# Performance work log

Measured on AMD Instinct MI355X. Metric: run time of the kernel, lower is better.

The kernel has to match this reference:

```python
import jax, jax.numpy as jnp
import numpy as np

N_NODES = 50000
N_EDGES = 800000
IN_FEATS = 128
OUT_FEATS = 64


def setup_inputs() -> dict:
    key = jax.random.key(0)
    k1, k2, k3, k4, k5, k6 = jax.random.split(key, 6)
    feat = jax.random.normal(k1, (N_NODES, IN_FEATS), dtype=jnp.float32)
    edge_src = jax.random.randint(k2, (N_EDGES,), 0, N_NODES, dtype=jnp.int64)
    edge_dst = jax.random.randint(k3, (N_EDGES,), 0, N_NODES, dtype=jnp.int64)
    eweight = jax.random.uniform(k4, (N_EDGES,), dtype=jnp.float32)
    W = jax.random.normal(k5, (OUT_FEATS, IN_FEATS), dtype=jnp.float32) * (1.0 / np.sqrt(IN_FEATS))
    b = jax.random.normal(k6, (OUT_FEATS,), dtype=jnp.float32) * 0.01
    return {"feat": feat, "edge_src": edge_src, "edge_dst": edge_dst,
            "eweight": eweight, "W": W, "b": b}


def reference(feat, edge_src, edge_dst, eweight, W, b):
    # Linear: [N, in] @ [in, out] + [out]
    h = jnp.einsum('ni,oi->no', feat, W) + b
    # u_mul_e: gather src features, scale by per-edge weight -> [E, out]
    m = h[edge_src] * eweight[:, None]
    # sum reduce over dst -> [N, out]
    out = jax.ops.segment_sum(m, edge_dst, num_segments=N_NODES)
    return out
```

## Files before the change

### kernel.cpp

```cpp
#include <hip/hip_runtime.h>

#define IN_FEATS 128
#define OUT_FEATS 64
#define TM 64
#define ALD 136
#define BW_LOG 6
#define BWIDTH 64
#define MAX_NB 1024
#define SE_PER_BLK 2048
#define MAX_BUCKET 3072

typedef short bf16x8 __attribute__((ext_vector_type(8)));
typedef float f32x4 __attribute__((ext_vector_type(4)));

__device__ inline unsigned short f2bf(float f) {
    unsigned u = __float_as_uint(f);
    u += 0x7FFFu + ((u >> 16) & 1u);
    return (unsigned short)(u >> 16);
}
__device__ inline float bf2f_lo(unsigned v) { return __uint_as_float(v << 16); }
__device__ inline float bf2f_hi(unsigned v) { return __uint_as_float(v & 0xFFFF0000u); }
__device__ inline ushort4 cvt4(float4 t) {
    ushort4 s; s.x = f2bf(t.x); s.y = f2bf(t.y); s.z = f2bf(t.z); s.w = f2bf(t.w);
    return s;
}

__global__ __launch_bounds__(256) void coarse_hist(
    const int* __restrict__ edst, int* __restrict__ ghist, int n_edges, int nb)
{
    __shared__ int hist[MAX_NB];
    const int tid = threadIdx.x;
    for (int i = tid; i < nb; i += 256) hist[i] = 0;
    __syncthreads();

    const int n4 = n_edges >> 2;
    const int4* ed4 = (const int4*)edst;
    for (int i = blockIdx.x * 256 + tid; i < n4; i += gridDim.x * 256) {
        int4 d = ed4[i];
        atomicAdd(&hist[d.x >> BW_LOG], 1);
        atomicAdd(&hist[d.y >> BW_LOG], 1);
        atomicAdd(&hist[d.z >> BW_LOG], 1);
        atomicAdd(&hist[d.w >> BW_LOG], 1);
    }
    if (blockIdx.x == 0 && tid < (n_edges & 3))
        atomicAdd(&hist[edst[n4 * 4 + tid] >> BW_LOG], 1);
    __syncthreads();
    for (int i = tid; i < nb; i += 256)
        if (hist[i]) atomicAdd(&ghist[i], hist[i]);
}

__global__ __launch_bounds__(256) void coarse_scan(
    const int* __restrict__ ghist, int* __restrict__ goff,
    int* __restrict__ gcur, int nb)
{
    __shared__ int wsum[4];
    __shared__ int wpre[4];
    const int tid  = threadIdx.x;
    const int lane = tid & 63;
    const int wv   = tid >> 6;
    int i0 = tid * 4;
    int v[4];
    int s = 0;
#pragma unroll
    for (int j = 0; j < 4; ++j) v[j] = (i0 + j < nb) ? ghist[i0 + j] : 0;
#pragma unroll
    for (int j = 0; j < 4; ++j) { int t = v[j]; v[j] = s; s += t; }
    int inc = s;
    for (int off = 1; off < 64; off <<= 1) {
        int t = __shfl_up(inc, off, 64);
        if (lane >= off) inc += t;
    }
    int wexcl = inc - s;
    if (lane == 63) wsum[wv] = inc;
    __syncthreads();
    if (tid == 0) {
        int a = 0;
        for (int k = 0; k < 4; ++k) { wpre[k] = a; a += wsum[k]; }
    }
    __syncthreads();
    int tbase = wpre[wv] + wexcl;
#pragma unroll
    for (int j = 0; j < 4; ++j) {
        int idx = i0 + j;
        if (idx < nb) { int e = tbase + v[j]; goff[idx] = e; gcur[idx] = e; }
    }
    if (tid == 0) goff[nb] = wpre[3] + wsum[3];
}

__global__ __launch_bounds__(256) void stage_linear(
    const float* __restrict__ feat, const float* __restrict__ W,
    const float* __restrict__ b, unsigned short* __restrict__ h,
    const int* __restrict__ esrc, const int* __restrict__ edst,
    const float* __restrict__ ew, int* __restrict__ gcur,
    int2* __restrict__ gstage, int n_nodes, int n_edges, int nb, int nstage)
{
    __shared__ union {
        struct { unsigned short As[TM * ALD]; unsigned short Ws[OUT_FEATS * ALD]; } lin;
        struct { int cnt[MAX_NB]; int base[MAX_NB]; } st;
    } sm;
    const int tid = threadIdx.x;

    if ((int)blockIdx.x < nstage) {
        int* cnt  = sm.st.cnt;
        int* base = sm.st.base;
        for (int i = tid; i < nb; i += 256) cnt[i] = 0;
        __syncthreads();

        const int e0 = blockIdx.x * SE_PER_BLK + tid * 8;
        int dk[8]; int sk[8]; float wk[8]; int bk[8]; int rk[8];
        if (e0 + 7 < n_edges) {
            *((int4*)&dk[0]) = *((const int4*)&edst[e0]);
            *((int4*)&dk[4]) = *((const int4*)&edst[e0 + 4]);
            *((int4*)&sk[0]) = *((const int4*)&esrc[e0]);
            *((int4*)&sk[4]) = *((const int4*)&esrc[e0 + 4]);
            *((float4*)&wk[0]) = *((const float4*)&ew[e0]);
            *((float4*)&wk[4]) = *((const float4*)&ew[e0 + 4]);
#pragma unroll
            for (int i = 0; i < 8; ++i) {
                bk[i] = dk[i] >> BW_LOG;
                rk[i] = atomicAdd(&cnt[bk[i]], 1);
            }
        } else {
#pragma unroll
            for (int i = 0; i < 8; ++i) {
                int e = e0 + i;
                if (e < n_edges) {
                    dk[i] = edst[e]; sk[i] = esrc[e]; wk[i] = ew[e];
                    bk[i] = dk[i] >> BW_LOG;
                    rk[i] = atomicAdd(&cnt[bk[i]], 1);
                } else bk[i] = -1;
            }
        }
        __syncthreads();
        for (int i = tid; i < nb; i += 256) {
            int c = cnt[i];
            base[i] = c ? atomicAdd(&gcur[i], c) : 0;
        }
        __syncthreads();
#pragma unroll
        for (int i = 0; i < 8; ++i) {
            if (bk[i] >= 0)
                gstage[base[bk[i]] + rk[i]] =
                    make_int2(((dk[i] & (BWIDTH - 1)) << 16) | sk[i],
                              __float_as_int(wk[i]));
        }
    } else {
        unsigned short* As = sm.lin.As;
        unsigned short* Ws = sm.lin.Ws;
        const int row0 = ((int)blockIdx.x - nstage) * TM;

        {
            const int c  = tid & 63;
            const int kb = (tid >> 6) * 32;
            const float4* wrow = (const float4*)(W + (size_t)c * IN_FEATS + kb);
#pragma unroll
            for (int i = 0; i < 8; ++i)
                *((ushort4*)&Ws[c * ALD + kb + i * 4]) = cvt4(wrow[i]);
        }
        {
#pragma unroll
            for (int i = 0; i < 8; ++i) {
                int flat = i * 256 + tid;
                int r  = flat >> 5;
                int kc = flat & 31;
                int gr = row0 + r;
                float4 t = (gr < n_nodes)
                    ? ((const float4*)(feat + (size_t)gr * IN_FEATS))[kc]
                    : make_float4(0.f, 0.f, 0.f, 0.f);
                *((ushort4*)&As[r * ALD + kc * 4]) = cvt4(t);
            }
        }
        __syncthreads();

        const int w    = tid >> 6;
        const int lane = tid & 63;
        const int m    = lane & 15;
        const int quad = lane >> 4;
        const int koff = quad * 8;

        f32x4 acc[4];
#pragma unroll
        for (int t = 0; t < 4; ++t) acc[t] = (f32x4){0.f, 0.f, 0.f, 0.f};

#pragma unroll
        for (int chunk = 0; chunk < 4; ++chunk) {
            const int kc = chunk * 32 + koff;
            bf16x8 a = *((const bf16x8*)&As[(w * 16 + m) * ALD + kc]);
#pragma unroll
            for (int t = 0; t < 4; ++t) {
                bf16x8 bfr = *((const bf16x8*)&Ws[(t * 16 + m) * ALD + kc]);
                acc[t] = __builtin_amdgcn_mfma_f32_16x16x32_bf16(a, bfr, acc[t], 0, 0, 0);
            }
        }

#pragma unroll
        for (int t = 0; t < 4; ++t) {
            const int col = t * 16 + m;
            const float bias = b[col];
#pragma unroll
            for (int i = 0; i < 4; ++i) {
                int r = row0 + w * 16 + quad * 4 + i;
                if (r < n_nodes)
                    h[(size_t)r * OUT_FEATS + col] = f2bf(acc[t][i] + bias);
            }
        }
    }
}

__global__ __launch_bounds__(256) void bin_sort(
    int2* __restrict__ gstage, const int* __restrict__ goff,
    int2* __restrict__ seg, int n_nodes, int nb)
{
    __shared__ int2 recs[MAX_BUCKET];
    __shared__ int cnt[BWIDTH];
    __shared__ int cur[BWIDTH];
    const int tid = threadIdx.x;
    const int b   = blockIdx.x;
    const int s0  = goff[b], s1 = goff[b + 1];
    const int m   = s1 - s0;

    if (tid < BWIDTH) cnt[tid] = 0;
    __syncthreads();

    for (int i = tid; i < m; i += 256) {
        int2 r = gstage[s0 + i];
        recs[i] = r;
        atomicAdd(&cnt[(r.x >> 16) & 63], 1);
    }
    __syncthreads();

    if (tid < 64) {
        int v = cnt[tid];
        int inc = v;
        for (int o = 1; o < 64; o <<= 1) {
            int t = __shfl_up(inc, o, 64);
            if (tid >= o) inc += t;
        }
        int excl = inc - v;
        cur[tid] = excl;
        int node = b * BWIDTH + tid;
        if (node < n_nodes) seg[node] = make_int2(s0 + excl, s0 + excl + v);
    }
    __syncthreads();

    for (int i = tid; i < m; i += 256) {
        int2 r = recs[i];
        int pos = atomicAdd(&cur[(r.x >> 16) & 63], 1);
        gstage[s0 + pos] = r;
    }
}

__global__ __launch_bounds__(256) void gather_kernel(
    const unsigned short* __restrict__ h, const int2* __restrict__ seg,
    const int2* __restrict__ perm2, float* __restrict__ out, int n_nodes)
{
    const int wid  = (blockIdx.x * blockDim.x + threadIdx.x) >> 6;
    const int lane = threadIdx.x & 63;
    const int g    = lane >> 5;
    const int f2   = lane & 31;
    const int node = wid * 2 + g;
    const unsigned* h32 = (const unsigned*)h;

    int2 se = (node < n_nodes) ? seg[node] : make_int2(0, 0);
    const int len = se.y - se.x;
    const int olen = __shfl_xor(len, 32, 64);
    const int omax = max(len, olen);

    float a0 = 0.f, a1 = 0.f;
    for (int u = 0; u < omax; u += 8) {
        int2 r[8]; unsigned hv[8];
#pragma unroll
        for (int k = 0; k < 8; ++k) {
            int uk  = u + k;
            int pos = (uk < len) ? (se.x + uk) : (len > 0 ? se.y - 1 : 0);
            r[k] = perm2[pos];
        }
#pragma unroll
        for (int k = 0; k < 8; ++k)
            hv[k] = h32[(size_t)(r[k].x & 0xFFFF) * 32 + f2];
#pragma unroll
        for (int k = 0; k < 8; ++k) {
            float w = (u + k < len) ? __int_as_float(r[k].y) : 0.f;
            a0 += w * bf2f_lo(hv[k]);
            a1 += w * bf2f_hi(hv[k]);
        }
    }
    if (node < n_nodes) {
        float2 o; o.x = a0; o.y = a1;
        *((float2*)&out[(size_t)node * OUT_FEATS + 2 * f2]) = o;
    }
}

__global__ __launch_bounds__(256) void scatter_kernel(
    const unsigned short* __restrict__ h, const int* __restrict__ esrc,
    const int* __restrict__ edst, const float* __restrict__ ew,
    float* __restrict__ out, int n_edges)
{
    const int lane = threadIdx.x & 63;
    const int wave = threadIdx.x >> 6;
    const int stride = gridDim.x * 4;
    for (int e = blockIdx.x * 4 + wave; e < n_edges; e += stride) {
        const int s = esrc[e];
        const int d = edst[e];
        const float w = ew[e];
        atomicAdd(out + (size_t)d * OUT_FEATS + lane,
                  bf2f_lo((unsigned)h[(size_t)s * OUT_FEATS + lane]) * w);
    }
}

extern "C" void kernel_launch(void* const* d_in, const int* in_sizes, int n_in,
                              void* d_out, int out_size, void* d_ws, size_t ws_size,
                              hipStream_t stream) {
    const float* feat = (const float*)d_in[0];
    const int*   esrc = (const int*)d_in[1];
    const int*   edst = (const int*)d_in[2];
    const float* ew   = (const float*)d_in[3];
    const float* W    = (const float*)d_in[4];
    const float* b    = (const float*)d_in[5];
    float* out = (float*)d_out;

    const int n_nodes = in_sizes[0] / IN_FEATS;
    const int n_edges = in_sizes[1];
    const int nb = (n_nodes + BWIDTH - 1) >> BW_LOG;
    const int nlin = (n_nodes + TM - 1) / TM;
    const int nstage = (n_edges + SE_PER_BLK - 1) / SE_PER_BLK;

    char* wsb = (char*)d_ws;
    unsigned short* h = (unsigned short*)wsb;
    size_t off_ghist = (((size_t)n_nodes * OUT_FEATS * sizeof(unsigned short)) + 15) & ~(size_t)15;
    size_t sz_ghist  = (((size_t)nb * sizeof(int)) + 15) & ~(size_t)15;
    size_t off_goff  = off_ghist + sz_ghist;
    size_t sz_goff   = (((size_t)(nb + 1) * sizeof(int)) + 15) & ~(size_t)15;
    size_t off_gcur  = off_goff + sz_goff;
    size_t sz_gcur   = (((size_t)nb * sizeof(int)) + 15) & ~(size_t)15;
    size_t off_seg   = off_gcur + sz_gcur;
    size_t sz_seg    = (((size_t)n_nodes * sizeof(int2)) + 15) & ~(size_t)15;
    size_t off_stage = off_seg + sz_seg;
    size_t needed    = off_stage + (size_t)n_edges * sizeof(int2);

    bool binnable = (nb <= MAX_NB) && (n_nodes < 65536) &&
                    ((size_t)n_edges / (size_t)nb * 2 + 256 <= MAX_BUCKET);

    if (ws_size >= needed && binnable) {
        int*  ghist  = (int*)(wsb + off_ghist);
        int*  goff   = (int*)(wsb + off_goff);
        int*  gcur   = (int*)(wsb + off_gcur);
        int2* seg    = (int2*)(wsb + off_seg);
        int2* gstage = (int2*)(wsb + off_stage);
        hipMemsetAsync(ghist, 0, (size_t)nb * sizeof(int), stream);
        coarse_hist<<<128, 256, 0, stream>>>(edst, ghist, n_edges, nb);
        coarse_scan<<<1, 256, 0, stream>>>(ghist, goff, gcur, nb);
        stage_linear<<<nstage + nlin, 256, 0, stream>>>(
            feat, W, b, h, esrc, edst, ew, gcur, gstage,
            n_nodes, n_edges, nb, nstage);
        bin_sort<<<nb, 256, 0, stream>>>(gstage, goff, seg, n_nodes, nb);
        const int gwaves = (n_nodes + 1) / 2;
        gather_kernel<<<(gwaves + 3) / 4, 256, 0, stream>>>(
            h, seg, gstage, out, n_nodes);
    } else {
        stage_linear<<<nlin, 256, 0, stream>>>(
            feat, W, b, h, esrc, edst, ew, nullptr, nullptr,
            n_nodes, n_edges, nb, 0);
        hipMemsetAsync(d_out, 0, (size_t)out_size * sizeof(float), stream);
        scatter_kernel<<<8192, 256, 0, stream>>>(h, esrc, edst, ew, out, n_edges);
    }
}
```

Measured before the change: 146.1 us.

## Fuse bucket sort and gather into one kernel using LDS-resident sorted edges

```diff
diff --git a/kernel.cpp b/kernel.cpp
--- a/kernel.cpp
+++ b/kernel.cpp
@@ -207,12 +207,14 @@
     }
 }
 
-__global__ __launch_bounds__(256) void bin_sort(
-    int2* __restrict__ gstage, const int* __restrict__ goff,
-    int2* __restrict__ seg, int n_nodes, int nb)
+__global__ __launch_bounds__(512) void sort_gather(
+    const unsigned short* __restrict__ h, const int* __restrict__ goff,
+    const int2* __restrict__ gstage, float* __restrict__ out, int n_nodes)
 {
     __shared__ int2 recs[MAX_BUCKET];
+    __shared__ int2 srec[MAX_BUCKET];
     __shared__ int cnt[BWIDTH];
+    __shared__ int cur0[BWIDTH];
     __shared__ int cur[BWIDTH];
     const int tid = threadIdx.x;
     const int b   = blockIdx.x;
@@ -222,7 +224,7 @@
     if (tid < BWIDTH) cnt[tid] = 0;
     __syncthreads();
 
-    for (int i = tid; i < m; i += 256) {
+    for (int i = tid; i < m; i += 512) {
         int2 r = gstage[s0 + i];
         recs[i] = r;
         atomicAdd(&cnt[(r.x >> 16) & 63], 1);
@@ -237,57 +239,58 @@
             if (tid >= o) inc += t;
         }
         int excl = inc - v;
-        cur[tid] = excl;
-        int node = b * BWIDTH + tid;
-        if (node < n_nodes) seg[node] = make_int2(s0 + excl, s0 + excl + v);
-    }
-    __syncthreads();
-
-    for (int i = tid; i < m; i += 256) {
+        cur0[tid] = excl;
+        cur[tid]  = excl;
+    }
+    __syncthreads();
+
+    for (int i = tid; i < m; i += 512) {
         int2 r = recs[i];
         int pos = atomicAdd(&cur[(r.x >> 16) & 63], 1);
-        gstage[s0 + pos] = r;
-    }
-}
-
-__global__ __launch_bounds__(256) void gather_kernel(
-    const unsigned short* __restrict__ h, const int2* __restrict__ seg,
-    const int2* __restrict__ perm2, float* __restrict__ out, int n_nodes)
-{
-    const int wid  = (blockIdx.x * blockDim.x + threadIdx.x) >> 6;
-    const int lane = threadIdx.x & 63;
-    const int g    = lane >> 5;
-    const int f2   = lane & 31;
-    const int node = wid * 2 + g;
-    const unsigned* h32 = (const unsigned*)h;
-
-    int2 se = (node < n_nodes) ? seg[node] : make_int2(0, 0);
-    const int len = se.y - se.x;
-    const int olen = __shfl_xor(len, 32, 64);
-    const int omax = max(len, olen);
-
-    float a0 = 0.f, a1 = 0.f;
-    for (int u = 0; u < omax; u += 8) {
-        int2 r[8]; unsigned hv[8];
-#pragma unroll
-        for (int k = 0; k < 8; ++k) {
-            int uk  = u + k;
-            int pos = (uk < len) ? (se.x + uk) : (len > 0 ? se.y - 1 : 0);
-            r[k] = perm2[pos];
-        }
-#pragma unroll
-        for (int k = 0; k < 8; ++k)
-            hv[k] = h32[(size_t)(r[k].x & 0xFFFF) * 32 + f2];
-#pragma unroll
-        for (int k = 0; k < 8; ++k) {
-            float w = (u + k < len) ? __int_as_float(r[k].y) : 0.f;
-            a0 += w * bf2f_lo(hv[k]);
-            a1 += w * bf2f_hi(hv[k]);
-        }
-    }
-    if (node < n_nodes) {
-        float2 o; o.x = a0; o.y = a1;
-        *((float2*)&out[(size_t)node * OUT_FEATS + 2 * f2]) = o;
+        srec[pos] = r;
+    }
+    __syncthreads();
+
+    const int lane = tid & 63;
+    const int wv   = tid >> 6;
+    const int g    = lane >> 4;
+    const int f4   = lane & 15;
+    const uint2* h64 = (const uint2*)h;
+
+#pragma unroll
+    for (int it = 0; it < 2; ++it) {
+        const int nl   = wv * 8 + it * 4 + g;
+        const int node = b * BWIDTH + nl;
+        const int st   = cur0[nl];
+        const int len  = cnt[nl];
+        int omax = len;
+        omax = max(omax, __shfl_xor(omax, 16, 64));
+        omax = max(omax, __shfl_xor(omax, 32, 64));
+
+        float a0 = 0.f, a1 = 0.f, a2 = 0.f, a3 = 0.f;
+        for (int u = 0; u < omax; u += 8) {
+            int2 r[8]; uint2 hv[8];
+#pragma unroll
+            for (int k = 0; k < 8; ++k) {
+                int uk = u + k;
+                r[k] = srec[(uk < len) ? (st + uk) : 0];
+            }
+#pragma unroll
+            for (int k = 0; k < 8; ++k)
+                hv[k] = h64[(size_t)(r[k].x & 0xFFFF) * 16 + f4];
+#pragma unroll
+            for (int k = 0; k < 8; ++k) {
+                float w = (u + k < len) ? __int_as_float(r[k].y) : 0.f;
+                a0 += w * bf2f_lo(hv[k].x);
+                a1 += w * bf2f_hi(hv[k].x);
+                a2 += w * bf2f_lo(hv[k].y);
+                a3 += w * bf2f_hi(hv[k].y);
+            }
+        }
+        if (node < n_nodes) {
+            float4 o; o.x = a0; o.y = a1; o.z = a2; o.w = a3;
+            *((float4*)&out[(size_t)node * OUT_FEATS + f4 * 4]) = o;
+        }
     }
 }
 
@@ -333,9 +336,7 @@
     size_t sz_goff   = (((size_t)(nb + 1) * sizeof(int)) + 15) & ~(size_t)15;
     size_t off_gcur  = off_goff + sz_goff;
     size_t sz_gcur   = (((size_t)nb * sizeof(int)) + 15) & ~(size_t)15;
-    size_t off_seg   = off_gcur + sz_gcur;
-    size_t sz_seg    = (((size_t)n_nodes * sizeof(int2)) + 15) & ~(size_t)15;
-    size_t off_stage = off_seg + sz_seg;
+    size_t off_stage = off_gcur + sz_gcur;
     size_t needed    = off_stage + (size_t)n_edges * sizeof(int2);
 
     bool binnable = (nb <= MAX_NB) && (n_nodes < 65536) &&
@@ -345,7 +346,6 @@
         int*  ghist  = (int*)(wsb + off_ghist);
         int*  goff   = (int*)(wsb + off_goff);
         int*  gcur   = (int*)(wsb + off_gcur);
-        int2* seg    = (int2*)(wsb + off_seg);
         int2* gstage = (int2*)(wsb + off_stage);
         hipMemsetAsync(ghist, 0, (size_t)nb * sizeof(int), stream);
         coarse_hist<<<128, 256, 0, stream>>>(edst, ghist, n_edges, nb);
@@ -353,10 +353,7 @@
         stage_linear<<<nstage + nlin, 256, 0, stream>>>(
             feat, W, b, h, esrc, edst, ew, gcur, gstage,
             n_nodes, n_edges, nb, nstage);
-        bin_sort<<<nb, 256, 0, stream>>>(gstage, goff, seg, n_nodes, nb);
-        const int gwaves = (n_nodes + 1) / 2;
-        gather_kernel<<<(gwaves + 3) / 4, 256, 0, stream>>>(
-            h, seg, gstage, out, n_nodes);
+        sort_gather<<<nb, 512, 0, stream>>>(h, goff, gstage, out, n_nodes);
     } else {
         stage_linear<<<nlin, 256, 0, stream>>>(
             feat, W, b, h, esrc, edst, ew, nullptr, nullptr,
```

Measured after the change: 137.1 us. -6.2%, faster.
